# Kernel tuning notes

Hardware: AMD Instinct MI355X
Metric: run time of the kernel (lower is better)

Reference implementation:

```python
import jax, jax.numpy as jnp
import numpy as np


def setup_inputs() -> dict:
    key = jax.random.key(0)
    ks = jax.random.split(key, 7)
    B, S, E, H, D = 4, 2048, 1024, 16, 64
    return {
        "q": jax.random.normal(ks[0], (B, S, E), dtype=jnp.float32),
        "k": jax.random.normal(ks[1], (B, S, E), dtype=jnp.float32),
        "v": jax.random.normal(ks[2], (B, S, E), dtype=jnp.float32),
        "Wq": jax.random.uniform(ks[3], (H, E, D), dtype=jnp.float32),
        "Wk": jax.random.uniform(ks[4], (H, E, D), dtype=jnp.float32),
        "Wv": jax.random.uniform(ks[5], (H, E, D), dtype=jnp.float32),
        "Wo": jax.random.uniform(ks[6], (H * D, E), dtype=jnp.float32),
    }


def reference(q, k, v, Wq, Wk, Wv, Wo):
    B, S, E = q.shape
    H, _, D = Wq.shape
    qh = jnp.einsum("bse,hed->bhsd", q, Wq)
    kh = jnp.einsum("bse,hed->bhsd", k, Wk)
    vh = jnp.einsum("bse,hed->bhsd", v, Wv)
    # Faithful quirk: original divides by C**(-0.5) -> multiplies by sqrt(D)
    scale = jnp.asarray(D, q.dtype) ** 0.5
    scores = jnp.einsum("bhsd,bhtd->bhst", qh, kh) * scale  # [B,H,S,S]
    causal = jnp.tril(jnp.ones((S, S), dtype=bool))
    scores = jnp.where(causal, scores, -jnp.inf)
    attn = jax.nn.softmax(scores, axis=-1)
    out_h = jnp.einsum("bhst,bhtd->bhsd", attn, vh)  # [B,H,S,D]
    concat = out_h.transpose(0, 2, 1, 3).reshape(B, S, H * D)
    return concat @ Wo
```

## Files before the change

### kernel.cpp

```cpp
#include <hip/hip_runtime.h>
#include <hip/hip_bf16.h>

#define B_ 4
#define S_ 2048
#define E_ 1024
#define H_ 16
#define D_ 64

typedef _Float16 f16;
typedef __attribute__((ext_vector_type(4))) float f32x4;
typedef __attribute__((ext_vector_type(8))) short bf16x8;
typedef __attribute__((ext_vector_type(8))) unsigned short u16x8;
typedef __attribute__((ext_vector_type(8))) _Float16 f16x8;
typedef __attribute__((ext_vector_type(4))) float float4v;

__device__ __forceinline__ unsigned short f2bf(float f) {
  union { float f; unsigned int u; } x; x.f = f;
  unsigned int u = x.u;
  u = (u + 0x7FFFu + ((u >> 16) & 1u)) >> 16;
  return (unsigned short)u;
}

#define MFMA_BF(a, b, c) __builtin_amdgcn_mfma_f32_16x16x32_bf16((a), (b), (c), 0, 0, 0)
#define MFMA_F16(a, b, c) __builtin_amdgcn_mfma_f32_16x16x32_f16((a), (b), (c), 0, 0, 0)

__global__ __launch_bounds__(256)
void transpose_convert(const float* __restrict__ src, unsigned short* __restrict__ dst,
                       int R, int C, float scale) {
  __shared__ unsigned short tile[64][65];
  const int rb = blockIdx.y * 64;
  const int cb = blockIdx.x * 64;
  const size_t mo = (size_t)blockIdx.z * (size_t)R * (size_t)C;
  const int t = threadIdx.x;
  const int r = t >> 2;
  const int c0 = (t & 3) * 16;
  const float* sp = src + mo + (size_t)(rb + r) * C + cb + c0;
#pragma unroll
  for (int j = 0; j < 16; j += 4) {
    float4v vv = *(const float4v*)(sp + j);
    tile[r][c0 + j + 0] = f2bf(vv[0] * scale);
    tile[r][c0 + j + 1] = f2bf(vv[1] * scale);
    tile[r][c0 + j + 2] = f2bf(vv[2] * scale);
    tile[r][c0 + j + 3] = f2bf(vv[3] * scale);
  }
  __syncthreads();
  u16x8 w0, w1;
#pragma unroll
  for (int j = 0; j < 8; ++j) w0[j] = tile[c0 + j][r];
#pragma unroll
  for (int j = 0; j < 8; ++j) w1[j] = tile[c0 + 8 + j][r];
  unsigned short* dp = dst + mo + (size_t)(cb + r) * R + rb + c0;
  *(u16x8*)(dp) = w0;
  *(u16x8*)(dp + 8) = w1;
}

__global__ __launch_bounds__(256)
void transpose_split_f16(const float* __restrict__ src, f16* __restrict__ dhi,
                         f16* __restrict__ dlo, int R, int C, float scale) {
  __shared__ float tile[64][65];
  const int rb = blockIdx.y * 64;
  const int cb = blockIdx.x * 64;
  const size_t mo = (size_t)blockIdx.z * (size_t)R * (size_t)C;
  const int t = threadIdx.x;
  const int r = t >> 2;
  const int c0 = (t & 3) * 16;
  const float* sp = src + mo + (size_t)(rb + r) * C + cb + c0;
#pragma unroll
  for (int j = 0; j < 16; j += 4) {
    float4v vv = *(const float4v*)(sp + j);
    tile[r][c0 + j + 0] = vv[0] * scale;
    tile[r][c0 + j + 1] = vv[1] * scale;
    tile[r][c0 + j + 2] = vv[2] * scale;
    tile[r][c0 + j + 3] = vv[3] * scale;
  }
  __syncthreads();
  f16x8 h0, h1, l0, l1;
#pragma unroll
  for (int j = 0; j < 8; ++j) {
    float x = tile[c0 + j][r];
    f16 hi = (f16)x;
    h0[j] = hi; l0[j] = (f16)(x - (float)hi);
  }
#pragma unroll
  for (int j = 0; j < 8; ++j) {
    float x = tile[c0 + 8 + j][r];
    f16 hi = (f16)x;
    h1[j] = hi; l1[j] = (f16)(x - (float)hi);
  }
  const size_t o = mo + (size_t)(cb + r) * R + rb + c0;
  *(f16x8*)(dhi + o) = h0; *(f16x8*)(dhi + o + 8) = h1;
  *(f16x8*)(dlo + o) = l0; *(f16x8*)(dlo + o + 8) = l1;
}

__global__ __launch_bounds__(256)
void proj_qk(const float* __restrict__ q, const float* __restrict__ k,
             const f16* __restrict__ Whi, const f16* __restrict__ Wlo,
             f16* __restrict__ out_hi, f16* __restrict__ out_lo) {
  __shared__ f16 Ah[128 * 32], Al[128 * 32];
  __shared__ f16 Bh[64 * 32], Bl[64 * 32];
  const int t = threadIdx.x;
  const int p = blockIdx.z >> 2;
  const int b = blockIdx.z & 3;
  const int h = blockIdx.y;
  const int s0 = blockIdx.x * 128;
  const float* X = p ? k : q;

  const int arow = t >> 1;
  const int ac0 = (t & 1) * 16;
  const float* aptr = X + ((size_t)b * S_ + s0 + arow) * E_ + ac0;

  const int brow = t >> 2;
  const int bc0 = (t & 3) * 8;
  const size_t wof = (((size_t)p * H_ + h) * D_ + brow) * E_ + bc0;

  const int w = t >> 6, l = t & 63, lr = l & 15, lg = l >> 4;

  f32x4 acc[2][4];
#pragma unroll
  for (int i = 0; i < 2; ++i)
#pragma unroll
    for (int c = 0; c < 4; ++c) acc[i][c] = (f32x4){0.f, 0.f, 0.f, 0.f};

  for (int e0 = 0; e0 < E_; e0 += 32) {
    __syncthreads();
    f16x8 h0, h1, l0, l1;
#pragma unroll
    for (int jj = 0; jj < 2; ++jj) {
      float4v va = *(const float4v*)(aptr + e0 + jj * 8);
      float4v vb = *(const float4v*)(aptr + e0 + jj * 8 + 4);
#pragma unroll
      for (int j = 0; j < 4; ++j) {
        f16 hi = (f16)va[j];
        (jj ? h1 : h0)[j] = hi;
        (jj ? l1 : l0)[j] = (f16)(va[j] - (float)hi);
      }
#pragma unroll
      for (int j = 0; j < 4; ++j) {
        f16 hi = (f16)vb[j];
        (jj ? h1 : h0)[4 + j] = hi;
        (jj ? l1 : l0)[4 + j] = (f16)(vb[j] - (float)hi);
      }
    }
    *(f16x8*)&Ah[arow * 32 + ac0] = h0; *(f16x8*)&Ah[arow * 32 + ac0 + 8] = h1;
    *(f16x8*)&Al[arow * 32 + ac0] = l0; *(f16x8*)&Al[arow * 32 + ac0 + 8] = l1;
    *(f16x8*)&Bh[brow * 32 + bc0] = *(const f16x8*)(Whi + wof + e0);
    *(f16x8*)&Bl[brow * 32 + bc0] = *(const f16x8*)(Wlo + wof + e0);
    __syncthreads();

    f16x8 ah0 = *(const f16x8*)&Ah[(w * 32 + lr) * 32 + lg * 8];
    f16x8 ah1 = *(const f16x8*)&Ah[(w * 32 + 16 + lr) * 32 + lg * 8];
    f16x8 al0 = *(const f16x8*)&Al[(w * 32 + lr) * 32 + lg * 8];
    f16x8 al1 = *(const f16x8*)&Al[(w * 32 + 16 + lr) * 32 + lg * 8];
#pragma unroll
    for (int c = 0; c < 4; ++c) {
      f16x8 bh = *(const f16x8*)&Bh[(c * 16 + lr) * 32 + lg * 8];
      f16x8 bl = *(const f16x8*)&Bl[(c * 16 + lr) * 32 + lg * 8];
      acc[0][c] = MFMA_F16(ah0, bh, acc[0][c]);
      acc[0][c] = MFMA_F16(ah0, bl, acc[0][c]);
      acc[0][c] = MFMA_F16(al0, bh, acc[0][c]);
      acc[1][c] = MFMA_F16(ah1, bh, acc[1][c]);
      acc[1][c] = MFMA_F16(ah1, bl, acc[1][c]);
      acc[1][c] = MFMA_F16(al1, bh, acc[1][c]);
    }
  }

  const size_t ob = (((size_t)p * B_ + b) * H_ + h) * (size_t)S_ * D_;
#pragma unroll
  for (int i = 0; i < 2; ++i)
#pragma unroll
    for (int c = 0; c < 4; ++c)
#pragma unroll
      for (int r = 0; r < 4; ++r) {
        const int row = w * 32 + i * 16 + lg * 4 + r;
        const int col = c * 16 + lr;
        float x = acc[i][c][r];
        f16 hi = (f16)x;
        out_hi[ob + (size_t)(s0 + row) * D_ + col] = hi;
        out_lo[ob + (size_t)(s0 + row) * D_ + col] = (f16)(x - (float)hi);
      }
}

__global__ __launch_bounds__(256)
void proj_v(const float* __restrict__ v, const unsigned short* __restrict__ Wt,
            f16* __restrict__ vht) {
  __shared__ unsigned short sm[8704];
  unsigned short* As = sm;
  unsigned short* Bs = sm + 4096;
  const int t = threadIdx.x;
  const int b = blockIdx.z;
  const int h = blockIdx.y;
  const int s0 = blockIdx.x * 128;

  const int arow = t >> 1;
  const int ac0 = (t & 1) * 16;
  const float* aptr = v + ((size_t)b * S_ + s0 + arow) * E_ + ac0;

  const int brow = t >> 2;
  const int bc0 = (t & 3) * 8;
  const unsigned short* bptr = Wt + ((size_t)h * D_ + brow) * E_ + bc0;

  const int w = t >> 6, l = t & 63, lr = l & 15, lg = l >> 4;

  f32x4 acc[2][4];
#pragma unroll
  for (int i = 0; i < 2; ++i)
#pragma unroll
    for (int c = 0; c < 4; ++c) acc[i][c] = (f32x4){0.f, 0.f, 0.f, 0.f};

  for (int e0 = 0; e0 < E_; e0 += 32) {
    __syncthreads();
    float4v v0 = *(const float4v*)(aptr + e0);
    float4v v1 = *(const float4v*)(aptr + e0 + 4);
    float4v v2 = *(const float4v*)(aptr + e0 + 8);
    float4v v3 = *(const float4v*)(aptr + e0 + 12);
    u16x8 w0, w1;
#pragma unroll
    for (int j = 0; j < 4; ++j) { w0[j] = f2bf(v0[j]); w0[4 + j] = f2bf(v1[j]); }
#pragma unroll
    for (int j = 0; j < 4; ++j) { w1[j] = f2bf(v2[j]); w1[4 + j] = f2bf(v3[j]); }
    *(u16x8*)&As[arow * 32 + ac0] = w0;
    *(u16x8*)&As[arow * 32 + ac0 + 8] = w1;
    *(u16x8*)&Bs[brow * 32 + bc0] = *(const u16x8*)(bptr + e0);
    __syncthreads();

    bf16x8 af0 = *(const bf16x8*)&As[(w * 32 + lr) * 32 + lg * 8];
    bf16x8 af1 = *(const bf16x8*)&As[(w * 32 + 16 + lr) * 32 + lg * 8];
#pragma unroll
    for (int c = 0; c < 4; ++c) {
      bf16x8 bf = *(const bf16x8*)&Bs[(c * 16 + lr) * 32 + lg * 8];
      acc[0][c] = MFMA_BF(af0, bf, acc[0][c]);
      acc[1][c] = MFMA_BF(af1, bf, acc[1][c]);
    }
  }

  const size_t bhD = ((size_t)b * H_ + h) * D_;
  __syncthreads();
  f16* Td = (f16*)sm;
#pragma unroll
  for (int i = 0; i < 2; ++i)
#pragma unroll
    for (int c = 0; c < 4; ++c)
#pragma unroll
      for (int r = 0; r < 4; ++r) {
        const int srow = w * 32 + i * 16 + lg * 4 + r;
        Td[(c * 16 + lr) * 136 + srow] = (f16)acc[i][c][r];
      }
  __syncthreads();
  const int dd = t >> 2;
  const int sc2 = (t & 3) * 32;
  f16* vp = vht + (bhD + dd) * S_ + s0 + sc2;
#pragma unroll
  for (int j = 0; j < 4; ++j)
    *(f16x8*)(vp + j * 8) = *(const f16x8*)&Td[dd * 136 + sc2 + j * 8];
}

__global__ __launch_bounds__(256, 2)
void attn_kernel(const f16* __restrict__ qhh, const f16* __restrict__ qhl,
                 const f16* __restrict__ khh, const f16* __restrict__ khl,
                 const f16* __restrict__ vht, unsigned short* __restrict__ ao) {
  __shared__ f16 Ksh[2][64 * 64];
  __shared__ f16 Ksl[2][64 * 64];
  __shared__ f16 Vts[2][64 * 64];
  __shared__ f16 Pls[4][32 * 64];
  const int t = threadIdx.x;
  const int b = blockIdx.z, h = blockIdx.y;
  const int w = t >> 6, l = t & 63, lr = l & 15, lg = l >> 4;
  const size_t bh = ((size_t)b * H_ + h) * S_;
  const size_t bhD = ((size_t)b * H_ + h) * D_;
  const int cr0 = t >> 3, cch = t & 7;
  const int cr1 = (t + 256) >> 3;
  const int coff = (cch * 16);

#pragma unroll
  for (int ph = 0; ph < 2; ++ph) {
    const int qt = ph ? (15 - (int)blockIdx.x) : (int)blockIdx.x;
    const int q0 = qt * 128;

    f16x8 qfh[2][2], qfl[2][2];
#pragma unroll
    for (int i = 0; i < 2; ++i) {
      const size_t qo = (bh + q0 + w * 32 + i * 16 + lr) * D_;
#pragma unroll
      for (int hf = 0; hf < 2; ++hf) {
        qfh[i][hf] = *(const f16x8*)(qhh + qo + hf * 32 + lg * 8);
        qfl[i][hf] = *(const f16x8*)(qhl + qo + hf * 32 + lg * 8);
      }
    }

    f32x4 acc[2][4];
#pragma unroll
    for (int i = 0; i < 2; ++i)
#pragma unroll
      for (int c = 0; c < 4; ++c) acc[i][c] = (f32x4){0.f, 0.f, 0.f, 0.f};
    float mx[2][4], ls[2][4];
#pragma unroll
    for (int i = 0; i < 2; ++i)
#pragma unroll
      for (int r = 0; r < 4; ++r) { mx[i][r] = -3.0e38f; ls[i][r] = 0.f; }

    const int wmax = q0 + w * 32 + 31;
    const int nkt = 2 * qt + 2;
    int cur = 0;

    {
      const f16* kbh = khh + bh * D_;
      const f16* kbl = khl + bh * D_;
      const f16* vb = vht + bhD * S_;
      f16x8 a0 = *(const f16x8*)(kbh + cr0 * 64 + cch * 8);
      f16x8 a1 = *(const f16x8*)(kbh + cr1 * 64 + cch * 8);
      f16x8 b0 = *(const f16x8*)(kbl + cr0 * 64 + cch * 8);
      f16x8 b1 = *(const f16x8*)(kbl + cr1 * 64 + cch * 8);
      f16x8 c0 = *(const f16x8*)(vb + (size_t)cr0 * S_ + cch * 8);
      f16x8 c1 = *(const f16x8*)(vb + (size_t)cr1 * S_ + cch * 8);
      const int o0 = coff ^ ((cr0 & 7) << 4);
      const int o1 = coff ^ ((cr1 & 7) << 4);
      *(f16x8*)((char*)Ksh[0] + cr0 * 128 + o0) = a0;
      *(f16x8*)((char*)Ksh[0] + cr1 * 128 + o1) = a1;
      *(f16x8*)((char*)Ksl[0] + cr0 * 128 + o0) = b0;
      *(f16x8*)((char*)Ksl[0] + cr1 * 128 + o1) = b1;
      *(f16x8*)((char*)Vts[0] + cr0 * 128 + o0) = c0;
      *(f16x8*)((char*)Vts[0] + cr1 * 128 + o1) = c1;
    }

    for (int kt = 0; kt < nkt; ++kt) {
      const int kt0 = kt * 64;
      __syncthreads();

      const bool pf = (kt + 1 < nkt);
      f16x8 ra0, ra1, rb0, rb1, rc0, rc1;
      if (pf) {
        const int n0 = kt0 + 64;
        const f16* kbh = khh + (bh + n0) * D_;
        const f16* kbl = khl + (bh + n0) * D_;
        const f16* vb = vht + bhD * S_ + n0;
        ra0 = *(const f16x8*)(kbh + cr0 * 64 + cch * 8);
        ra1 = *(const f16x8*)(kbh + cr1 * 64 + cch * 8);
        rb0 = *(const f16x8*)(kbl + cr0 * 64 + cch * 8);
        rb1 = *(const f16x8*)(kbl + cr1 * 64 + cch * 8);
        rc0 = *(const f16x8*)(vb + (size_t)cr0 * S_ + cch * 8);
        rc1 = *(const f16x8*)(vb + (size_t)cr1 * S_ + cch * 8);
      }

      if (kt0 <= wmax) {
        f32x4 sc[2][4];
#pragma unroll
        for (int n = 0; n < 4; ++n) {
          const int krow = n * 16 + lr;
          const int sw = (krow & 7) << 4;
          const char* kb = (const char*)Ksh[cur] + krow * 128;
          const char* kbl2 = (const char*)Ksl[cur] + krow * 128;
          f16x8 kh0 = *(const f16x8*)(kb + ((lg * 16) ^ sw));
          f16x8 kh1 = *(const f16x8*)(kb + ((64 + lg * 16) ^ sw));
          f16x8 kl0 = *(const f16x8*)(kbl2 + ((lg * 16) ^ sw));
          f16x8 kl1 = *(const f16x8*)(kbl2 + ((64 + lg * 16) ^ sw));
#pragma unroll
          for (int i = 0; i < 2; ++i) {
            f32x4 z = (f32x4){0.f, 0.f, 0.f, 0.f};
            z = MFMA_F16(qfh[i][0], kh0, z);
            z = MFMA_F16(qfh[i][1], kh1, z);
            z = MFMA_F16(qfh[i][0], kl0, z);
            z = MFMA_F16(qfh[i][1], kl1, z);
            z = MFMA_F16(qfl[i][0], kh0, z);
            z = MFMA_F16(qfl[i][1], kh1, z);
            sc[i][n] = z;
          }
        }

#pragma unroll
        for (int i = 0; i < 2; ++i) {
          const int qbase = q0 + w * 32 + i * 16;
          const bool full = (kt0 + 63 <= qbase);
#pragma unroll
          for (int r = 0; r < 4; ++r) {
            const int qrow = qbase + lg * 4 + r;
            float v0 = sc[i][0][r], v1 = sc[i][1][r], v2 = sc[i][2][r], v3 = sc[i][3][r];
            if (!full) {
              v0 = (kt0 + 0 + lr <= qrow) ? v0 : -3.0e38f;
              v1 = (kt0 + 16 + lr <= qrow) ? v1 : -3.0e38f;
              v2 = (kt0 + 32 + lr <= qrow) ? v2 : -3.0e38f;
              v3 = (kt0 + 48 + lr <= qrow) ? v3 : -3.0e38f;
            }
            float tm = fmaxf(fmaxf(v0, v1), fmaxf(v2, v3));
            tm = fmaxf(tm, __shfl_xor(tm, 1));
            tm = fmaxf(tm, __shfl_xor(tm, 2));
            tm = fmaxf(tm, __shfl_xor(tm, 4));
            tm = fmaxf(tm, __shfl_xor(tm, 8));
            const float mn = fmaxf(mx[i][r], tm);
            const float corr = __expf(mx[i][r] - mn);
            mx[i][r] = mn;
            float p0 = __expf(v0 - mn), p1 = __expf(v1 - mn);
            float p2 = __expf(v2 - mn), p3 = __expf(v3 - mn);
            float ps = (p0 + p1) + (p2 + p3);
            ps += __shfl_xor(ps, 1);
            ps += __shfl_xor(ps, 2);
            ps += __shfl_xor(ps, 4);
            ps += __shfl_xor(ps, 8);
            ls[i][r] = ls[i][r] * corr + ps;
#pragma unroll
            for (int c = 0; c < 4; ++c) acc[i][c][r] *= corr;
            const int qi = i * 16 + lg * 4 + r;
            char* pb = (char*)&Pls[w][0] + qi * 128;
            const int sw2 = (qi & 7) << 4;
            *(f16*)(pb + ((0 + lr * 2) ^ sw2)) = (f16)p0;
            *(f16*)(pb + ((32 + lr * 2) ^ sw2)) = (f16)p1;
            *(f16*)(pb + ((64 + lr * 2) ^ sw2)) = (f16)p2;
            *(f16*)(pb + ((96 + lr * 2) ^ sw2)) = (f16)p3;
          }
        }

#pragma unroll
        for (int ks = 0; ks < 2; ++ks) {
          const int co = (ks * 64 + lg * 16);
          f16x8 pf0 = *(const f16x8*)((const char*)&Pls[w][0] + lr * 128 + (co ^ ((lr & 7) << 4)));
          f16x8 pf1 = *(const f16x8*)((const char*)&Pls[w][0] + (16 + lr) * 128 + (co ^ ((lr & 7) << 4)));
#pragma unroll
          for (int c = 0; c < 4; ++c) {
            const int vr = c * 16 + lr;
            f16x8 vf = *(const f16x8*)((const char*)Vts[cur] + vr * 128 + (co ^ ((vr & 7) << 4)));
            acc[0][c] = MFMA_F16(pf0, vf, acc[0][c]);
            acc[1][c] = MFMA_F16(pf1, vf, acc[1][c]);
          }
        }
      }

      __syncthreads();
      if (pf) {
        const int nb = cur ^ 1;
        const int o0 = coff ^ ((cr0 & 7) << 4);
        const int o1 = coff ^ ((cr1 & 7) << 4);
        *(f16x8*)((char*)Ksh[nb] + cr0 * 128 + o0) = ra0;
        *(f16x8*)((char*)Ksh[nb] + cr1 * 128 + o1) = ra1;
        *(f16x8*)((char*)Ksl[nb] + cr0 * 128 + o0) = rb0;
        *(f16x8*)((char*)Ksl[nb] + cr1 * 128 + o1) = rb1;
        *(f16x8*)((char*)Vts[nb] + cr0 * 128 + o0) = rc0;
        *(f16x8*)((char*)Vts[nb] + cr1 * 128 + o1) = rc1;
      }
      cur ^= 1;
    }

#pragma unroll
    for (int i = 0; i < 2; ++i)
#pragma unroll
      for (int r = 0; r < 4; ++r) {
        const float inv = 1.0f / ls[i][r];
        const size_t s = q0 + w * 32 + i * 16 + lg * 4 + r;
        const size_t o = ((size_t)b * S_ + s) * (H_ * D_) + (size_t)h * D_;
#pragma unroll
        for (int c = 0; c < 4; ++c)
          ao[o + c * 16 + lr] = f2bf(acc[i][c][r] * inv);
      }
  }
}

__global__ __launch_bounds__(256)
void out_gemm(const unsigned short* __restrict__ A, const unsigned short* __restrict__ Bt,
              float* __restrict__ Cout) {
  __shared__ unsigned short As[128 * 32];
  __shared__ unsigned short Bs[64 * 32];
  const int t = threadIdx.x;
  const int m0 = blockIdx.x * 128;
  const int n0 = blockIdx.y * 64;
  const int arow = t >> 1, ac0 = (t & 1) * 16;
  const unsigned short* aptr = A + (size_t)(m0 + arow) * 1024 + ac0;
  const int brow = t >> 2, bc0 = (t & 3) * 8;
  const unsigned short* bptr = Bt + (size_t)(n0 + brow) * 1024 + bc0;
  const int w = t >> 6, l = t & 63, lr = l & 15, lg = l >> 4;

  f32x4 acc[2][4];
#pragma unroll
  for (int i = 0; i < 2; ++i)
#pragma unroll
    for (int c = 0; c < 4; ++c) acc[i][c] = (f32x4){0.f, 0.f, 0.f, 0.f};

  for (int k0 = 0; k0 < 1024; k0 += 32) {
    __syncthreads();
    *(u16x8*)&As[arow * 32 + ac0] = *(const u16x8*)(aptr + k0);
    *(u16x8*)&As[arow * 32 + ac0 + 8] = *(const u16x8*)(aptr + k0 + 8);
    *(u16x8*)&Bs[brow * 32 + bc0] = *(const u16x8*)(bptr + k0);
    __syncthreads();

    bf16x8 af0 = *(const bf16x8*)&As[(w * 32 + lr) * 32 + lg * 8];
    bf16x8 af1 = *(const bf16x8*)&As[(w * 32 + 16 + lr) * 32 + lg * 8];
#pragma unroll
    for (int c = 0; c < 4; ++c) {
      bf16x8 bf = *(const bf16x8*)&Bs[(c * 16 + lr) * 32 + lg * 8];
      acc[0][c] = MFMA_BF(af0, bf, acc[0][c]);
      acc[1][c] = MFMA_BF(af1, bf, acc[1][c]);
    }
  }

#pragma unroll
  for (int i = 0; i < 2; ++i)
#pragma unroll
    for (int c = 0; c < 4; ++c)
#pragma unroll
      for (int r = 0; r < 4; ++r) {
        const int row = m0 + w * 32 + i * 16 + lg * 4 + r;
        const int col = n0 + c * 16 + lr;
        Cout[(size_t)row * 1024 + col] = acc[i][c][r];
      }
}

extern "C" void kernel_launch(void* const* d_in, const int* in_sizes, int n_in,
                              void* d_out, int out_size, void* d_ws, size_t ws_size,
                              hipStream_t stream) {
  const float* q = (const float*)d_in[0];
  const float* k = (const float*)d_in[1];
  const float* v = (const float*)d_in[2];
  const float* Wq = (const float*)d_in[3];
  const float* Wk = (const float*)d_in[4];
  const float* Wv = (const float*)d_in[5];
  const float* Wo = (const float*)d_in[6];

  const size_t NBH = (size_t)B_ * H_ * S_ * D_;
  const size_t WSZ = (size_t)H_ * D_ * E_;

  char* wsb = (char*)d_ws;
  f16* qk_hi = (f16*)wsb;
  f16* qk_lo = qk_hi + 2 * NBH;
  f16* vht = qk_lo + 2 * NBH;
  unsigned short* ao = (unsigned short*)(vht + NBH);
  f16* Wqk_hi = (f16*)(ao + NBH);
  f16* Wqk_lo = Wqk_hi + 2 * WSZ;
  unsigned short* Wvt = (unsigned short*)(Wqk_lo + 2 * WSZ);
  unsigned short* Wot = Wvt + WSZ;

  dim3 blk(256);
  transpose_split_f16<<<dim3(1, 16, 16), blk, 0, stream>>>(Wq, Wqk_hi, Wqk_lo, E_, D_, 8.0f);
  transpose_split_f16<<<dim3(1, 16, 16), blk, 0, stream>>>(Wk, Wqk_hi + WSZ, Wqk_lo + WSZ, E_, D_, 1.0f);
  transpose_convert<<<dim3(1, 16, 16), blk, 0, stream>>>(Wv, Wvt, E_, D_, 1.0f);
  transpose_convert<<<dim3(16, 16, 1), blk, 0, stream>>>(Wo, Wot, E_, E_, 1.0f);
  proj_qk<<<dim3(S_ / 128, H_, 8), blk, 0, stream>>>(q, k, Wqk_hi, Wqk_lo, qk_hi, qk_lo);
  proj_v<<<dim3(S_ / 128, H_, B_), blk, 0, stream>>>(v, Wvt, vht);
  attn_kernel<<<dim3(S_ / 256, H_, B_), blk, 0, stream>>>(
      qk_hi, qk_lo, qk_hi + NBH, qk_lo + NBH, vht, ao);
  out_gemm<<<dim3((B_ * S_) / 128, E_ / 64), blk, 0, stream>>>(ao, Wot, (float*)d_out);
}
```

Measured before the change: 515.5 us.

## Pre-convert inputs and use 128x128 register-prefetched GEMM tiles for projections

Input activations are converted once to f16 hi/lo or bf16 by separate prep kernels, so the projection GEMMs no longer redo the conversion for every head. The q/k/v projections and the output GEMM are rebuilt as full 128x128 tile GEMMs over all heads at once, each wave owning a 64x64 block, with padded LDS rows and register prefetch of the next K slice. This raises MFMA work per loaded byte and cuts redundant activation reads. The cost is extra kernel launches, intermediate buffers written and re-read through global memory, and larger register use per thread.

New measurement: 498.7 us. 3.3% less time.

```diff
diff --git a/kernel.cpp b/kernel.cpp
--- a/kernel.cpp
+++ b/kernel.cpp
@@ -6,6 +6,7 @@
 #define E_ 1024
 #define H_ 16
 #define D_ 64
+#define LDW 40
 
 typedef _Float16 f16;
 typedef __attribute__((ext_vector_type(4))) float f32x4;
@@ -93,165 +94,260 @@
 }
 
 __global__ __launch_bounds__(256)
-void proj_qk(const float* __restrict__ q, const float* __restrict__ k,
-             const f16* __restrict__ Whi, const f16* __restrict__ Wlo,
-             f16* __restrict__ out_hi, f16* __restrict__ out_lo) {
-  __shared__ f16 Ah[128 * 32], Al[128 * 32];
-  __shared__ f16 Bh[64 * 32], Bl[64 * 32];
+void prep_split(const float* __restrict__ x, f16* __restrict__ xh, f16* __restrict__ xl) {
+  const size_t i = ((size_t)blockIdx.x * 256 + threadIdx.x) * 8;
+  float4v a = *(const float4v*)(x + i);
+  float4v b = *(const float4v*)(x + i + 4);
+  f16x8 h, lo;
+#pragma unroll
+  for (int j = 0; j < 4; ++j) {
+    f16 hi = (f16)a[j]; h[j] = hi; lo[j] = (f16)(a[j] - (float)hi);
+  }
+#pragma unroll
+  for (int j = 0; j < 4; ++j) {
+    f16 hi = (f16)b[j]; h[4 + j] = hi; lo[4 + j] = (f16)(b[j] - (float)hi);
+  }
+  *(f16x8*)(xh + i) = h;
+  *(f16x8*)(xl + i) = lo;
+}
+
+__global__ __launch_bounds__(256)
+void prep_bf16(const float* __restrict__ x, unsigned short* __restrict__ xo) {
+  const size_t i = ((size_t)blockIdx.x * 256 + threadIdx.x) * 8;
+  float4v a = *(const float4v*)(x + i);
+  float4v b = *(const float4v*)(x + i + 4);
+  u16x8 o;
+#pragma unroll
+  for (int j = 0; j < 4; ++j) { o[j] = f2bf(a[j]); o[4 + j] = f2bf(b[j]); }
+  *(u16x8*)(xo + i) = o;
+}
+
+__global__ __launch_bounds__(256, 2)
+void proj_qk2(const f16* __restrict__ xh, const f16* __restrict__ xl,
+              const f16* __restrict__ Wh, const f16* __restrict__ Wl,
+              f16* __restrict__ out_hi, f16* __restrict__ out_lo) {
+  __shared__ f16 Ah[128 * LDW], Al[128 * LDW], Bh[128 * LDW], Bl[128 * LDW];
   const int t = threadIdx.x;
-  const int p = blockIdx.z >> 2;
-  const int b = blockIdx.z & 3;
-  const int h = blockIdx.y;
-  const int s0 = blockIdx.x * 128;
-  const float* X = p ? k : q;
-
-  const int arow = t >> 1;
-  const int ac0 = (t & 1) * 16;
-  const float* aptr = X + ((size_t)b * S_ + s0 + arow) * E_ + ac0;
-
-  const int brow = t >> 2;
-  const int bc0 = (t & 3) * 8;
-  const size_t wof = (((size_t)p * H_ + h) * D_ + brow) * E_ + bc0;
-
+  const int m0 = blockIdx.x * 128, n0 = blockIdx.y * 128;
   const int w = t >> 6, l = t & 63, lr = l & 15, lg = l >> 4;
-
-  f32x4 acc[2][4];
-#pragma unroll
-  for (int i = 0; i < 2; ++i)
-#pragma unroll
-    for (int c = 0; c < 4; ++c) acc[i][c] = (f32x4){0.f, 0.f, 0.f, 0.f};
-
-  for (int e0 = 0; e0 < E_; e0 += 32) {
+  const int wm = (w & 1) * 64, wn = (w >> 1) * 64;
+
+  const int sr0 = t >> 2, sc = (t & 3) * 8;
+  const f16* gAh = xh + (size_t)(m0 + sr0) * 1024 + sc;
+  const f16* gAl = xl + (size_t)(m0 + sr0) * 1024 + sc;
+  const f16* gBh = Wh + (size_t)(n0 + sr0) * 1024 + sc;
+  const f16* gBl = Wl + (size_t)(n0 + sr0) * 1024 + sc;
+  const size_t rstep = (size_t)64 * 1024;
+  const int l0 = sr0 * LDW + sc, l1 = (sr0 + 64) * LDW + sc;
+
+  f32x4 acc[4][4];
+#pragma unroll
+  for (int im = 0; im < 4; ++im)
+#pragma unroll
+    for (int in = 0; in < 4; ++in) acc[im][in] = (f32x4){0.f, 0.f, 0.f, 0.f};
+
+  f16x8 r0 = *(const f16x8*)(gAh),         r1 = *(const f16x8*)(gAh + rstep);
+  f16x8 r2 = *(const f16x8*)(gAl),         r3 = *(const f16x8*)(gAl + rstep);
+  f16x8 r4 = *(const f16x8*)(gBh),         r5 = *(const f16x8*)(gBh + rstep);
+  f16x8 r6 = *(const f16x8*)(gBl),         r7 = *(const f16x8*)(gBl + rstep);
+  *(f16x8*)&Ah[l0] = r0; *(f16x8*)&Ah[l1] = r1;
+  *(f16x8*)&Al[l0] = r2; *(f16x8*)&Al[l1] = r3;
+  *(f16x8*)&Bh[l0] = r4; *(f16x8*)&Bh[l1] = r5;
+  *(f16x8*)&Bl[l0] = r6; *(f16x8*)&Bl[l1] = r7;
+
+  for (int k0 = 0; k0 < 1024; k0 += 32) {
     __syncthreads();
-    f16x8 h0, h1, l0, l1;
-#pragma unroll
-    for (int jj = 0; jj < 2; ++jj) {
-      float4v va = *(const float4v*)(aptr + e0 + jj * 8);
-      float4v vb = *(const float4v*)(aptr + e0 + jj * 8 + 4);
-#pragma unroll
-      for (int j = 0; j < 4; ++j) {
-        f16 hi = (f16)va[j];
-        (jj ? h1 : h0)[j] = hi;
-        (jj ? l1 : l0)[j] = (f16)(va[j] - (float)hi);
-      }
-#pragma unroll
-      for (int j = 0; j < 4; ++j) {
-        f16 hi = (f16)vb[j];
-        (jj ? h1 : h0)[4 + j] = hi;
-        (jj ? l1 : l0)[4 + j] = (f16)(vb[j] - (float)hi);
-      }
-    }
-    *(f16x8*)&Ah[arow * 32 + ac0] = h0; *(f16x8*)&Ah[arow * 32 + ac0 + 8] = h1;
-    *(f16x8*)&Al[arow * 32 + ac0] = l0; *(f16x8*)&Al[arow * 32 + ac0 + 8] = l1;
-    *(f16x8*)&Bh[brow * 32 + bc0] = *(const f16x8*)(Whi + wof + e0);
-    *(f16x8*)&Bl[brow * 32 + bc0] = *(const f16x8*)(Wlo + wof + e0);
+    const bool pf = (k0 + 32 < 1024);
+    if (pf) {
+      r0 = *(const f16x8*)(gAh + k0 + 32); r1 = *(const f16x8*)(gAh + rstep + k0 + 32);
+      r2 = *(const f16x8*)(gAl + k0 + 32); r3 = *(const f16x8*)(gAl + rstep + k0 + 32);
+      r4 = *(const f16x8*)(gBh + k0 + 32); r5 = *(const f16x8*)(gBh + rstep + k0 + 32);
+      r6 = *(const f16x8*)(gBl + k0 + 32); r7 = *(const f16x8*)(gBl + rstep + k0 + 32);
+    }
+    f16x8 afh[4], afl[4], bfh[4], bfl[4];
+#pragma unroll
+    for (int im = 0; im < 4; ++im) {
+      afh[im] = *(const f16x8*)&Ah[(wm + im * 16 + lr) * LDW + lg * 8];
+      afl[im] = *(const f16x8*)&Al[(wm + im * 16 + lr) * LDW + lg * 8];
+    }
+#pragma unroll
+    for (int in = 0; in < 4; ++in) {
+      bfh[in] = *(const f16x8*)&Bh[(wn + in * 16 + lr) * LDW + lg * 8];
+      bfl[in] = *(const f16x8*)&Bl[(wn + in * 16 + lr) * LDW + lg * 8];
+    }
+#pragma unroll
+    for (int im = 0; im < 4; ++im)
+#pragma unroll
+      for (int in = 0; in < 4; ++in) {
+        acc[im][in] = MFMA_F16(afh[im], bfh[in], acc[im][in]);
+        acc[im][in] = MFMA_F16(afh[im], bfl[in], acc[im][in]);
+        acc[im][in] = MFMA_F16(afl[im], bfh[in], acc[im][in]);
+      }
     __syncthreads();
-
-    f16x8 ah0 = *(const f16x8*)&Ah[(w * 32 + lr) * 32 + lg * 8];
-    f16x8 ah1 = *(const f16x8*)&Ah[(w * 32 + 16 + lr) * 32 + lg * 8];
-    f16x8 al0 = *(const f16x8*)&Al[(w * 32 + lr) * 32 + lg * 8];
-    f16x8 al1 = *(const f16x8*)&Al[(w * 32 + 16 + lr) * 32 + lg * 8];
-#pragma unroll
-    for (int c = 0; c < 4; ++c) {
-      f16x8 bh = *(const f16x8*)&Bh[(c * 16 + lr) * 32 + lg * 8];
-      f16x8 bl = *(const f16x8*)&Bl[(c * 16 + lr) * 32 + lg * 8];
-      acc[0][c] = MFMA_F16(ah0, bh, acc[0][c]);
-      acc[0][c] = MFMA_F16(ah0, bl, acc[0][c]);
-      acc[0][c] = MFMA_F16(al0, bh, acc[0][c]);
-      acc[1][c] = MFMA_F16(ah1, bh, acc[1][c]);
-      acc[1][c] = MFMA_F16(ah1, bl, acc[1][c]);
-      acc[1][c] = MFMA_F16(al1, bh, acc[1][c]);
-    }
-  }
-
-  const size_t ob = (((size_t)p * B_ + b) * H_ + h) * (size_t)S_ * D_;
-#pragma unroll
-  for (int i = 0; i < 2; ++i)
-#pragma unroll
-    for (int c = 0; c < 4; ++c)
-#pragma unroll
-      for (int r = 0; r < 4; ++r) {
-        const int row = w * 32 + i * 16 + lg * 4 + r;
-        const int col = c * 16 + lr;
-        float x = acc[i][c][r];
-        f16 hi = (f16)x;
-        out_hi[ob + (size_t)(s0 + row) * D_ + col] = hi;
-        out_lo[ob + (size_t)(s0 + row) * D_ + col] = (f16)(x - (float)hi);
-      }
-}
-
-__global__ __launch_bounds__(256)
-void proj_v(const float* __restrict__ v, const unsigned short* __restrict__ Wt,
-            f16* __restrict__ vht) {
-  __shared__ unsigned short sm[8704];
-  unsigned short* As = sm;
-  unsigned short* Bs = sm + 4096;
+    if (pf) {
+      *(f16x8*)&Ah[l0] = r0; *(f16x8*)&Ah[l1] = r1;
+      *(f16x8*)&Al[l0] = r2; *(f16x8*)&Al[l1] = r3;
+      *(f16x8*)&Bh[l0] = r4; *(f16x8*)&Bh[l1] = r5;
+      *(f16x8*)&Bl[l0] = r6; *(f16x8*)&Bl[l1] = r7;
+    }
+  }
+
+  const int b = m0 >> 11, s0b = m0 & 2047;
+#pragma unroll
+  for (int im = 0; im < 4; ++im)
+#pragma unroll
+    for (int in = 0; in < 4; ++in)
+#pragma unroll
+      for (int rr = 0; rr < 4; ++rr) {
+        const int srow = s0b + wm + im * 16 + lg * 4 + rr;
+        const int n = n0 + wn + in * 16 + lr;
+        const int h = n >> 6, d = n & 63;
+        const size_t o = (((size_t)b * H_ + h) * S_ + srow) * D_ + d;
+        const float x = acc[im][in][rr];
+        const f16 hi = (f16)x;
+        out_hi[o] = hi;
+        out_lo[o] = (f16)(x - (float)hi);
+      }
+}
+
+__global__ __launch_bounds__(256, 2)
+void proj_v2(const unsigned short* __restrict__ xv, const unsigned short* __restrict__ Wv,
+             f16* __restrict__ vht) {
+  __shared__ short smem[17408];
+  unsigned short* As = (unsigned short*)smem;
+  unsigned short* Bs = As + 128 * LDW;
   const int t = threadIdx.x;
-  const int b = blockIdx.z;
-  const int h = blockIdx.y;
-  const int s0 = blockIdx.x * 128;
-
-  const int arow = t >> 1;
-  const int ac0 = (t & 1) * 16;
-  const float* aptr = v + ((size_t)b * S_ + s0 + arow) * E_ + ac0;
-
-  const int brow = t >> 2;
-  const int bc0 = (t & 3) * 8;
-  const unsigned short* bptr = Wt + ((size_t)h * D_ + brow) * E_ + bc0;
-
+  const int m0 = blockIdx.x * 128, n0 = blockIdx.y * 128;
   const int w = t >> 6, l = t & 63, lr = l & 15, lg = l >> 4;
-
-  f32x4 acc[2][4];
-#pragma unroll
-  for (int i = 0; i < 2; ++i)
-#pragma unroll
-    for (int c = 0; c < 4; ++c) acc[i][c] = (f32x4){0.f, 0.f, 0.f, 0.f};
-
-  for (int e0 = 0; e0 < E_; e0 += 32) {
+  const int wm = (w & 1) * 64, wn = (w >> 1) * 64;
+
+  const int sr0 = t >> 2, sc = (t & 3) * 8;
+  const unsigned short* gA = xv + (size_t)(m0 + sr0) * 1024 + sc;
+  const unsigned short* gB = Wv + (size_t)(n0 + sr0) * 1024 + sc;
+  const size_t rstep = (size_t)64 * 1024;
+  const int l0 = sr0 * LDW + sc, l1 = (sr0 + 64) * LDW + sc;
+
+  f32x4 acc[4][4];
+#pragma unroll
+  for (int im = 0; im < 4; ++im)
+#pragma unroll
+    for (int in = 0; in < 4; ++in) acc[im][in] = (f32x4){0.f, 0.f, 0.f, 0.f};
+
+  u16x8 r0 = *(const u16x8*)(gA), r1 = *(const u16x8*)(gA + rstep);
+  u16x8 r2 = *(const u16x8*)(gB), r3 = *(const u16x8*)(gB + rstep);
+  *(u16x8*)&As[l0] = r0; *(u16x8*)&As[l1] = r1;
+  *(u16x8*)&Bs[l0] = r2; *(u16x8*)&Bs[l1] = r3;
+
+  for (int k0 = 0; k0 < 1024; k0 += 32) {
     __syncthreads();
-    float4v v0 = *(const float4v*)(aptr + e0);
-    float4v v1 = *(const float4v*)(aptr + e0 + 4);
-    float4v v2 = *(const float4v*)(aptr + e0 + 8);
-    float4v v3 = *(const float4v*)(aptr + e0 + 12);
-    u16x8 w0, w1;
-#pragma unroll
-    for (int j = 0; j < 4; ++j) { w0[j] = f2bf(v0[j]); w0[4 + j] = f2bf(v1[j]); }
-#pragma unroll
-    for (int j = 0; j < 4; ++j) { w1[j] = f2bf(v2[j]); w1[4 + j] = f2bf(v3[j]); }
-    *(u16x8*)&As[arow * 32 + ac0] = w0;
-    *(u16x8*)&As[arow * 32 + ac0 + 8] = w1;
-    *(u16x8*)&Bs[brow * 32 + bc0] = *(const u16x8*)(bptr + e0);
+    const bool pf = (k0 + 32 < 1024);
+    if (pf) {
+      r0 = *(const u16x8*)(gA + k0 + 32); r1 = *(const u16x8*)(gA + rstep + k0 + 32);
+      r2 = *(const u16x8*)(gB + k0 + 32); r3 = *(const u16x8*)(gB + rstep + k0 + 32);
+    }
+    bf16x8 af[4], bf[4];
+#pragma unroll
+    for (int im = 0; im < 4; ++im)
+      af[im] = *(const bf16x8*)&As[(wm + im * 16 + lr) * LDW + lg * 8];
+#pragma unroll
+    for (int in = 0; in < 4; ++in)
+      bf[in] = *(const bf16x8*)&Bs[(wn + in * 16 + lr) * LDW + lg * 8];
+#pragma unroll
+    for (int im = 0; im < 4; ++im)
+#pragma unroll
+      for (int in = 0; in < 4; ++in)
+        acc[im][in] = MFMA_BF(af[im], bf[in], acc[im][in]);
     __syncthreads();
-
-    bf16x8 af0 = *(const bf16x8*)&As[(w * 32 + lr) * 32 + lg * 8];
-    bf16x8 af1 = *(const bf16x8*)&As[(w * 32 + 16 + lr) * 32 + lg * 8];
-#pragma unroll
-    for (int c = 0; c < 4; ++c) {
-      bf16x8 bf = *(const bf16x8*)&Bs[(c * 16 + lr) * 32 + lg * 8];
-      acc[0][c] = MFMA_BF(af0, bf, acc[0][c]);
-      acc[1][c] = MFMA_BF(af1, bf, acc[1][c]);
-    }
-  }
-
-  const size_t bhD = ((size_t)b * H_ + h) * D_;
+    if (pf) {
+      *(u16x8*)&As[l0] = r0; *(u16x8*)&As[l1] = r1;
+      *(u16x8*)&Bs[l0] = r2; *(u16x8*)&Bs[l1] = r3;
+    }
+  }
+
   __syncthreads();
-  f16* Td = (f16*)sm;
-#pragma unroll
-  for (int i = 0; i < 2; ++i)
-#pragma unroll
-    for (int c = 0; c < 4; ++c)
-#pragma unroll
-      for (int r = 0; r < 4; ++r) {
-        const int srow = w * 32 + i * 16 + lg * 4 + r;
-        Td[(c * 16 + lr) * 136 + srow] = (f16)acc[i][c][r];
+  f16* Td = (f16*)smem;
+#pragma unroll
+  for (int im = 0; im < 4; ++im)
+#pragma unroll
+    for (int in = 0; in < 4; ++in)
+#pragma unroll
+      for (int rr = 0; rr < 4; ++rr) {
+        const int srow = wm + im * 16 + lg * 4 + rr;
+        const int ncol = wn + in * 16 + lr;
+        Td[ncol * 136 + srow] = (f16)acc[im][in][rr];
       }
   __syncthreads();
-  const int dd = t >> 2;
-  const int sc2 = (t & 3) * 32;
-  f16* vp = vht + (bhD + dd) * S_ + s0 + sc2;
-#pragma unroll
-  for (int j = 0; j < 4; ++j)
-    *(f16x8*)(vp + j * 8) = *(const f16x8*)&Td[dd * 136 + sc2 + j * 8];
+  const int n = t >> 1, sc2 = (t & 1) * 64;
+  const int b = m0 >> 11, s0b = m0 & 2047;
+  const int h = (n0 + n) >> 6, d = (n0 + n) & 63;
+  f16* vp = vht + (((size_t)b * H_ + h) * D_ + d) * S_ + s0b + sc2;
+#pragma unroll
+  for (int j = 0; j < 8; ++j)
+    *(f16x8*)(vp + j * 8) = *(const f16x8*)&Td[n * 136 + sc2 + j * 8];
+}
+
+__global__ __launch_bounds__(256, 2)
+void out_gemm2(const unsigned short* __restrict__ A, const unsigned short* __restrict__ Bt,
+               float* __restrict__ Cout) {
+  __shared__ unsigned short As[128 * LDW], Bs[128 * LDW];
+  const int t = threadIdx.x;
+  const int m0 = blockIdx.x * 128, n0 = blockIdx.y * 128;
+  const int w = t >> 6, l = t & 63, lr = l & 15, lg = l >> 4;
+  const int wm = (w & 1) * 64, wn = (w >> 1) * 64;
+
+  const int sr0 = t >> 2, sc = (t & 3) * 8;
+  const unsigned short* gA = A + (size_t)(m0 + sr0) * 1024 + sc;
+  const unsigned short* gB = Bt + (size_t)(n0 + sr0) * 1024 + sc;
+  const size_t rstep = (size_t)64 * 1024;
+  const int l0 = sr0 * LDW + sc, l1 = (sr0 + 64) * LDW + sc;
+
+  f32x4 acc[4][4];
+#pragma unroll
+  for (int im = 0; im < 4; ++im)
+#pragma unroll
+    for (int in = 0; in < 4; ++in) acc[im][in] = (f32x4){0.f, 0.f, 0.f, 0.f};
+
+  u16x8 r0 = *(const u16x8*)(gA), r1 = *(const u16x8*)(gA + rstep);
+  u16x8 r2 = *(const u16x8*)(gB), r3 = *(const u16x8*)(gB + rstep);
+  *(u16x8*)&As[l0] = r0; *(u16x8*)&As[l1] = r1;
+  *(u16x8*)&Bs[l0] = r2; *(u16x8*)&Bs[l1] = r3;
+
+  for (int k0 = 0; k0 < 1024; k0 += 32) {
+    __syncthreads();
+    const bool pf = (k0 + 32 < 1024);
+    if (pf) {
+      r0 = *(const u16x8*)(gA + k0 + 32); r1 = *(const u16x8*)(gA + rstep + k0 + 32);
+      r2 = *(const u16x8*)(gB + k0 + 32); r3 = *(const u16x8*)(gB + rstep + k0 + 32);
+    }
+    bf16x8 af[4], bf[4];
+#pragma unroll
+    for (int im = 0; im < 4; ++im)
+      af[im] = *(const bf16x8*)&As[(wm + im * 16 + lr) * LDW + lg * 8];
+#pragma unroll
+    for (int in = 0; in < 4; ++in)
+      bf[in] = *(const bf16x8*)&Bs[(wn + in * 16 + lr) * LDW + lg * 8];
+#pragma unroll
+    for (int im = 0; im < 4; ++im)
+#pragma unroll
+      for (int in = 0; in < 4; ++in)
+        acc[im][in] = MFMA_BF(af[im], bf[in], acc[im][in]);
+    __syncthreads();
+    if (pf) {
+      *(u16x8*)&As[l0] = r0; *(u16x8*)&As[l1] = r1;
+      *(u16x8*)&Bs[l0] = r2; *(u16x8*)&Bs[l1] = r3;
+    }
+  }
+
+#pragma unroll
+  for (int im = 0; im < 4; ++im)
+#pragma unroll
+    for (int in = 0; in < 4; ++in)
+#pragma unroll
+      for (int rr = 0; rr < 4; ++rr) {
+        const int row = m0 + wm + im * 16 + lg * 4 + rr;
+        const int col = n0 + wn + in * 16 + lr;
+        Cout[(size_t)row * 1024 + col] = acc[im][in][rr];
+      }
 }
 
 __global__ __launch_bounds__(256, 2)
@@ -452,55 +548,6 @@
   }
 }
 
-__global__ __launch_bounds__(256)
-void out_gemm(const unsigned short* __restrict__ A, const unsigned short* __restrict__ Bt,
-              float* __restrict__ Cout) {
-  __shared__ unsigned short As[128 * 32];
-  __shared__ unsigned short Bs[64 * 32];
-  const int t = threadIdx.x;
-  const int m0 = blockIdx.x * 128;
-  const int n0 = blockIdx.y * 64;
-  const int arow = t >> 1, ac0 = (t & 1) * 16;
-  const unsigned short* aptr = A + (size_t)(m0 + arow) * 1024 + ac0;
-  const int brow = t >> 2, bc0 = (t & 3) * 8;
-  const unsigned short* bptr = Bt + (size_t)(n0 + brow) * 1024 + bc0;
-  const int w = t >> 6, l = t & 63, lr = l & 15, lg = l >> 4;
-
-  f32x4 acc[2][4];
-#pragma unroll
-  for (int i = 0; i < 2; ++i)
-#pragma unroll
-    for (int c = 0; c < 4; ++c) acc[i][c] = (f32x4){0.f, 0.f, 0.f, 0.f};
-
-  for (int k0 = 0; k0 < 1024; k0 += 32) {
-    __syncthreads();
-    *(u16x8*)&As[arow * 32 + ac0] = *(const u16x8*)(aptr + k0);
-    *(u16x8*)&As[arow * 32 + ac0 + 8] = *(const u16x8*)(aptr + k0 + 8);
-    *(u16x8*)&Bs[brow * 32 + bc0] = *(const u16x8*)(bptr + k0);
-    __syncthreads();
-
-    bf16x8 af0 = *(const bf16x8*)&As[(w * 32 + lr) * 32 + lg * 8];
-    bf16x8 af1 = *(const bf16x8*)&As[(w * 32 + 16 + lr) * 32 + lg * 8];
-#pragma unroll
-    for (int c = 0; c < 4; ++c) {
-      bf16x8 bf = *(const bf16x8*)&Bs[(c * 16 + lr) * 32 + lg * 8];
-      acc[0][c] = MFMA_BF(af0, bf, acc[0][c]);
-      acc[1][c] = MFMA_BF(af1, bf, acc[1][c]);
-    }
-  }
-
-#pragma unroll
-  for (int i = 0; i < 2; ++i)
-#pragma unroll
-    for (int c = 0; c < 4; ++c)
-#pragma unroll
-      for (int r = 0; r < 4; ++r) {
-        const int row = m0 + w * 32 + i * 16 + lg * 4 + r;
-        const int col = n0 + c * 16 + lr;
-        Cout[(size_t)row * 1024 + col] = acc[i][c][r];
-      }
-}
-
 extern "C" void kernel_launch(void* const* d_in, const int* in_sizes, int n_in,
                               void* d_out, int out_size, void* d_ws, size_t ws_size,
                               hipStream_t stream) {
@@ -516,23 +563,32 @@
   const size_t WSZ = (size_t)H_ * D_ * E_;
 
   char* wsb = (char*)d_ws;
-  f16* qk_hi = (f16*)wsb;
-  f16* qk_lo = qk_hi + 2 * NBH;
-  f16* vht = qk_lo + 2 * NBH;
-  unsigned short* ao = (unsigned short*)(vht + NBH);
-  f16* Wqk_hi = (f16*)(ao + NBH);
+  f16* Wqk_hi = (f16*)wsb;
   f16* Wqk_lo = Wqk_hi + 2 * WSZ;
   unsigned short* Wvt = (unsigned short*)(Wqk_lo + 2 * WSZ);
   unsigned short* Wot = Wvt + WSZ;
+  f16* qk_hi = (f16*)(wsb + (size_t)12 * 1024 * 1024);
+  f16* qk_lo = qk_hi + 2 * NBH;
+  char* flex = wsb + (size_t)76 * 1024 * 1024;
+  f16* xh = (f16*)flex;
+  f16* xl = (f16*)(flex + (size_t)16 * 1024 * 1024);
+  unsigned short* xv = (unsigned short*)flex;
+  f16* vht = (f16*)(flex + (size_t)16 * 1024 * 1024);
+  unsigned short* ao = (unsigned short*)flex;
 
   dim3 blk(256);
   transpose_split_f16<<<dim3(1, 16, 16), blk, 0, stream>>>(Wq, Wqk_hi, Wqk_lo, E_, D_, 8.0f);
   transpose_split_f16<<<dim3(1, 16, 16), blk, 0, stream>>>(Wk, Wqk_hi + WSZ, Wqk_lo + WSZ, E_, D_, 1.0f);
   transpose_convert<<<dim3(1, 16, 16), blk, 0, stream>>>(Wv, Wvt, E_, D_, 1.0f);
   transpose_convert<<<dim3(16, 16, 1), blk, 0, stream>>>(Wo, Wot, E_, E_, 1.0f);
-  proj_qk<<<dim3(S_ / 128, H_, 8), blk, 0, stream>>>(q, k, Wqk_hi, Wqk_lo, qk_hi, qk_lo);
-  proj_v<<<dim3(S_ / 128, H_, B_), blk, 0, stream>>>(v, Wvt, vht);
+  prep_split<<<dim3(4096), blk, 0, stream>>>(q, xh, xl);
+  proj_qk2<<<dim3(64, 8), blk, 0, stream>>>(xh, xl, Wqk_hi, Wqk_lo, qk_hi, qk_lo);
+  prep_split<<<dim3(4096), blk, 0, stream>>>(k, xh, xl);
+  proj_qk2<<<dim3(64, 8), blk, 0, stream>>>(xh, xl, Wqk_hi + WSZ, Wqk_lo + WSZ,
+                                            qk_hi + NBH, qk_lo + NBH);
+  prep_bf16<<<dim3(4096), blk, 0, stream>>>(v, xv);
+  proj_v2<<<dim3(64, 8), blk, 0, stream>>>(xv, Wvt, vht);
   attn_kernel<<<dim3(S_ / 256, H_, B_), blk, 0, stream>>>(
       qk_hi, qk_lo, qk_hi + NBH, qk_lo + NBH, vht, ao);
-  out_gemm<<<dim3((B_ * S_) / 128, E_ / 64), blk, 0, stream>>>(ao, Wot, (float*)d_out);
-}
+  out_gemm2<<<dim3(64, 8), blk, 0, stream>>>(ao, Wot, (float*)d_out);
+}
```
